# Performance work log

Measured on AMD Instinct MI355X. Metric: run time of the kernel, lower is better.

## Reference

```python
import jax, jax.numpy as jnp
import numpy as np

B, L, D_MODEL = 4, 2048, 256
D_STATE, D_CONV, EXPAND = 16, 4, 2
D_INNER = EXPAND * D_MODEL          # 512
DT_RANK = (D_MODEL + 15) // 16      # 16
HORIZON = 96


def setup_inputs() -> dict:
    key = jax.random.key(0)
    ks = jax.random.split(key, 8)
    s = lambda k, shape, scale=0.02: jax.random.normal(k, shape, dtype=jnp.float32) * scale
    return {
        "x": jax.random.normal(ks[0], (B, L, D_MODEL), dtype=jnp.float32),
        "in_proj_w": s(ks[1], (2 * D_INNER, D_MODEL)),          # no bias (mamba default)
        "conv_w": s(ks[2], (D_INNER, 1, D_CONV), 0.1),          # depthwise causal conv
        "conv_b": jnp.zeros((D_INNER,), jnp.float32),
        "x_proj_w": s(ks[3], (DT_RANK + 2 * D_STATE, D_INNER)),
        "dt_proj_w": s(ks[4], (D_INNER, DT_RANK), 0.1),
        # softplus^{-1}(0.01): typical small initial dt
        "dt_proj_b": jnp.log(jnp.expm1(jnp.full((D_INNER,), 0.01, jnp.float32))),
        "A_log": jnp.log(jnp.broadcast_to(jnp.arange(1, D_STATE + 1, dtype=jnp.float32), (D_INNER, D_STATE))),
        "D_param": jnp.ones((D_INNER,), jnp.float32),
        "out_proj_w": s(ks[5], (D_MODEL, D_INNER)),
        "head_w": s(ks[6], (HORIZON, D_MODEL)),
        "head_b": jnp.zeros((HORIZON,), jnp.float32),
    }


def _silu(x):
    return x * jax.nn.sigmoid(x)


def _forward(x, in_proj_w, conv_w, conv_b, x_proj_w, dt_proj_w, dt_proj_b,
             A_log, D_param, out_proj_w, head_w, head_b):
    # in_proj -> split into conv/ssm branch and gate z
    xz = x @ in_proj_w.T                      # (B, L, 2*d_inner)
    x_in, z = jnp.split(xz, 2, axis=-1)
    # depthwise causal conv over time
    x_t = jnp.transpose(x_in, (0, 2, 1))      # (B, d_inner, L)
    x_conv = jax.lax.conv_general_dilated(
        x_t, conv_w, (1,), [(D_CONV - 1, 0)],
        feature_group_count=D_INNER, dimension_numbers=("NCH", "OIH", "NCH"))
    u = _silu(jnp.transpose(x_conv + conv_b[None, :, None], (0, 2, 1)))  # (B, L, d_inner)
    # input-dependent dt, B, C
    x_dbl = u @ x_proj_w.T
    dt, Bm, Cm = jnp.split(x_dbl, [DT_RANK, DT_RANK + D_STATE], axis=-1)
    delta = jax.nn.softplus(dt @ dt_proj_w.T + dt_proj_b)  # (B, L, d_inner)
    A = -jnp.exp(A_log)                                     # (d_inner, d_state)
    deltaA = jnp.exp(delta[..., None] * A)                  # (B, L, d_inner, d_state)
    deltaBu = delta[..., None] * Bm[:, :, None, :] * u[..., None]

    def step(h, ins):
        dA, dBu, c = ins                                    # (B,d,n),(B,d,n),(B,n)
        h = dA * h + dBu
        y = jnp.einsum("bdn,bn->bd", h, c)
        return h, y

    h0 = jnp.zeros((x.shape[0], D_INNER, D_STATE), x.dtype)
    xs = (jnp.moveaxis(deltaA, 1, 0), jnp.moveaxis(deltaBu, 1, 0), jnp.moveaxis(Cm, 1, 0))
    _, ys = jax.lax.scan(step, h0, xs)                      # (L, B, d_inner)
    y = jnp.moveaxis(ys, 0, 1) + u * D_param
    y = y * _silu(z)
    out = y @ out_proj_w.T                                  # (B, L, d_model)
    last = out[:, -1, :]
    return last @ head_w.T + head_b                         # (B, HORIZON)


def reference(x, in_proj_w, conv_w, conv_b, x_proj_w, dt_proj_w, dt_proj_b,
              A_log, D_param, out_proj_w, head_w, head_b):
    return _forward(x, in_proj_w, conv_w, conv_b, x_proj_w, dt_proj_w, dt_proj_b,
                    A_log, D_param, out_proj_w, head_w, head_b)
```

## Files before the change

### kernel.cpp

```cpp
#include <hip/hip_runtime.h>
#include <math.h>

#define BATCH 4
#define LSEQ 2048
#define BL (BATCH*LSEQ)
#define DMODEL 256
#define DINNER 512
#define NSTATE 16
#define DTRANK 16
#define NPROJ 48
#define HORIZ 96
#define NCH 32
#define TCH (LSEQ/NCH)

typedef __attribute__((ext_vector_type(8))) short short8b;
typedef __attribute__((ext_vector_type(4))) short short4b;
typedef __attribute__((ext_vector_type(4))) float f32x4;

__device__ __forceinline__ unsigned short f2bf(float f) {
  unsigned u = __float_as_uint(f);
  u += 0x7FFF + ((u >> 16) & 1);
  return (unsigned short)(u >> 16);
}
__device__ __forceinline__ float bf2f(unsigned short h) {
  return __uint_as_float(((unsigned)h) << 16);
}

__global__ __launch_bounds__(512) void k_front(const float* __restrict__ X,
                                               const float* __restrict__ W,
                                               const float* __restrict__ cw,
                                               const float* __restrict__ cb,
                                               const float* __restrict__ xpw,
                                               const float* __restrict__ opw,
                                               const float* __restrict__ hw,
                                               float* __restrict__ uT,
                                               float* __restrict__ dbl,
                                               float* __restrict__ hwf) {
  __shared__ unsigned short sBX[32*48*8];
  __shared__ unsigned short sAW[2*4*128*8];
  __shared__ float u_lds[128*36];
  const int tid = threadIdx.x;
  const int btc = blockIdx.x;
  if (btc >= 256) {
    const int fid = btc - 256;
    const int k0 = fid * 8;
    float* scratch = u_lds;
    {
      int m = tid >> 1;
      int half = (tid & 1) << 2;
      *(float4*)&scratch[m * 8 + half] =
        *(const float4*)&opw[(size_t)m * DINNER + k0 + half];
    }
    __syncthreads();
    for (int u = tid; u < HORIZ * 8; u += 512) {
      int t = u >> 3, kk = u & 7;
      const float* hr = &hw[(size_t)t * DMODEL];
      float acc = 0.f;
      #pragma unroll 8
      for (int m = 0; m < DMODEL; ++m) acc = fmaf(hr[m], scratch[m*8 + kk], acc);
      hwf[(size_t)t * DINNER + k0 + kk] = acc;
    }
    return;
  }
  const int bt0 = btc * 32;
  const bool edge0 = ((bt0 & (LSEQ - 1)) == 0);
  const int lane = tid & 63;
  const int w  = tid >> 6;
  const int fl = lane & 15;
  const int fg = lane >> 4;
  for (int u = tid; u < 1536; u += 512) {
    int tok = u >> 5, ko = u & 31;
    int g = bt0 - 16 + tok;
    if (g < 0) g = 0;
    const float* xr = &X[(size_t)g * DMODEL + ko * 8];
    float4 a = *(const float4*)xr, b = *(const float4*)(xr + 4);
    unsigned short t8[8] = {f2bf(a.x), f2bf(a.y), f2bf(a.z), f2bf(a.w),
                            f2bf(b.x), f2bf(b.y), f2bf(b.z), f2bf(b.w)};
    *(short8b*)&sBX[(ko * 48 + tok) * 8] = *(short8b*)t8;
  }
  float facc[4] = {0.f, 0.f, 0.f, 0.f};
  const int xo = tid >> 3;
  const int xt = (tid & 7) * 4;
  const int sj = tid >> 2;
  const int sk = tid & 3;
  for (int jc = 0; jc < 4; ++jc) {
    const int jbase = jc * 128;
    __syncthreads();
    {
      const float* wr = &W[(size_t)(jbase + sj) * DMODEL + sk * 8];
      float4 a = *(const float4*)wr, b = *(const float4*)(wr + 4);
      unsigned short t8[8] = {f2bf(a.x), f2bf(a.y), f2bf(a.z), f2bf(a.w),
                              f2bf(b.x), f2bf(b.y), f2bf(b.z), f2bf(b.w)};
      *(short8b*)&sAW[(sk * 128 + sj) * 8] = *(short8b*)t8;
    }
    __syncthreads();
    f32x4 acc0 = {0,0,0,0}, acc1 = {0,0,0,0}, acc2 = {0,0,0,0};
    for (int ks = 0; ks < 8; ++ks) {
      const int buf = ks & 1;
      if (ks < 7) {
        const float* wr = &W[(size_t)(jbase + sj) * DMODEL + (ks + 1) * 32 + sk * 8];
        float4 a = *(const float4*)wr, b = *(const float4*)(wr + 4);
        unsigned short t8[8] = {f2bf(a.x), f2bf(a.y), f2bf(a.z), f2bf(a.w),
                                f2bf(b.x), f2bf(b.y), f2bf(b.z), f2bf(b.w)};
        *(short8b*)&sAW[((buf ^ 1) * 512 + sk * 128 + sj) * 8] = *(short8b*)t8;
      }
      short8b aw = *(short8b*)&sAW[(buf * 512 + fg * 128 + w * 16 + fl) * 8];
      short8b x0 = *(short8b*)&sBX[((ks * 4 + fg) * 48 + fl) * 8];
      short8b x1 = *(short8b*)&sBX[((ks * 4 + fg) * 48 + 16 + fl) * 8];
      short8b x2 = *(short8b*)&sBX[((ks * 4 + fg) * 48 + 32 + fl) * 8];
      acc0 = __builtin_amdgcn_mfma_f32_16x16x32_bf16(x0, aw, acc0, 0, 0, 0);
      acc1 = __builtin_amdgcn_mfma_f32_16x16x32_bf16(x1, aw, acc1, 0, 0, 0);
      acc2 = __builtin_amdgcn_mfma_f32_16x16x32_bf16(x2, aw, acc2, 0, 0, 0);
      __syncthreads();
    }
    if (edge0) acc0 = (f32x4){0,0,0,0};
    const int j = jbase + w * 16 + fl;
    const float4 cwv = *(const float4*)&cw[j * 4];
    const float cbv = cb[j];
    float u1[4], u2[4];
    {
      float s3a = __shfl(acc1[3], lane - 16), s3b = __shfl(acc0[3], lane + 48);
      float s2a = __shfl(acc1[2], lane - 16), s2b = __shfl(acc0[2], lane + 48);
      float s1a = __shfl(acc1[1], lane - 16), s1b = __shfl(acc0[1], lane + 48);
      float p1 = fg ? s3a : s3b, p2 = fg ? s2a : s2b, p3 = fg ? s1a : s1b;
      float xm1[4] = {p1, acc1[0], acc1[1], acc1[2]};
      float xm2[4] = {p2, p1, acc1[0], acc1[1]};
      float xm3[4] = {p3, p2, p1, acc1[0]};
      #pragma unroll
      for (int r = 0; r < 4; ++r) {
        float s = cbv;
        s = fmaf(cwv.x, xm3[r], s); s = fmaf(cwv.y, xm2[r], s);
        s = fmaf(cwv.z, xm1[r], s); s = fmaf(cwv.w, acc1[r], s);
        u1[r] = s / (1.f + __expf(-s));
      }
    }
    {
      float s3a = __shfl(acc2[3], lane - 16), s3b = __shfl(acc1[3], lane + 48);
      float s2a = __shfl(acc2[2], lane - 16), s2b = __shfl(acc1[2], lane + 48);
      float s1a = __shfl(acc2[1], lane - 16), s1b = __shfl(acc1[1], lane + 48);
      float p1 = fg ? s3a : s3b, p2 = fg ? s2a : s2b, p3 = fg ? s1a : s1b;
      float xm1[4] = {p1, acc2[0], acc2[1], acc2[2]};
      float xm2[4] = {p2, p1, acc2[0], acc2[1]};
      float xm3[4] = {p3, p2, p1, acc2[0]};
      #pragma unroll
      for (int r = 0; r < 4; ++r) {
        float s = cbv;
        s = fmaf(cwv.x, xm3[r], s); s = fmaf(cwv.y, xm2[r], s);
        s = fmaf(cwv.z, xm1[r], s); s = fmaf(cwv.w, acc2[r], s);
        u2[r] = s / (1.f + __expf(-s));
      }
    }
    {
      const int jl = w * 16 + fl;
      #pragma unroll
      for (int r = 0; r < 4; ++r) {
        u_lds[jl * 36 + fg * 4 + r]      = u1[r];
        u_lds[jl * 36 + 16 + fg * 4 + r] = u2[r];
      }
    }
    __syncthreads();
    unsigned short* sw2 = sAW;
    for (int u = tid; u < 1536; u += 512) {
      int o = u >> 5, k4 = (u & 31) * 4;
      float4 v = *(const float4*)&xpw[(size_t)o * DINNER + jbase + k4];
      unsigned short t4[4] = {f2bf(v.x), f2bf(v.y), f2bf(v.z), f2bf(v.w)};
      *(short4b*)&sw2[o * 136 + k4] = *(short4b*)t4;
    }
    {
      const int tq = sk * 8;
      float4 a = *(float4*)&u_lds[sj * 36 + tq];
      float4 b = *(float4*)&u_lds[sj * 36 + tq + 4];
      *(float4*)&uT[(size_t)(jbase + sj) * BL + bt0 + tq]     = a;
      *(float4*)&uT[(size_t)(jbase + sj) * BL + bt0 + tq + 4] = b;
    }
    __syncthreads();
    if (tid < 384) {
      #pragma unroll 4
      for (int k = 0; k < 128; ++k) {
        float wv = bf2f(sw2[xo * 136 + k]);
        float4 uv = *(float4*)&u_lds[k * 36 + xt];
        facc[0] = fmaf(uv.x, wv, facc[0]);
        facc[1] = fmaf(uv.y, wv, facc[1]);
        facc[2] = fmaf(uv.z, wv, facc[2]);
        facc[3] = fmaf(uv.w, wv, facc[3]);
      }
    }
  }
  if (tid < 384) {
    #pragma unroll
    for (int i = 0; i < 4; ++i)
      dbl[(size_t)(bt0 + xt + i) * NPROJ + xo] = facc[i];
  }
}

__global__ __launch_bounds__(256) void k_scan(const float* __restrict__ uT,
                                              const float* __restrict__ dbl,
                                              const float* __restrict__ dtw,
                                              const float* __restrict__ dtb,
                                              const float* __restrict__ Alog,
                                              float* __restrict__ aprod,
                                              float* __restrict__ hacc) {
  __shared__ float sdt[64][17];
  __shared__ float sB[64][16];
  __shared__ float sdp[16][66][2];
  __shared__ float su[16][68];
  __shared__ float sdtw[16][17];
  __shared__ float sdtb[16];
  const int dblk = blockIdx.x, c = blockIdx.y, b = blockIdx.z;
  const int tid = threadIdx.x;
  const int d0 = dblk * 16;
  const int bt0 = b * LSEQ + c * TCH;
  {
    int tok = tid >> 2, q = (tid & 3) << 2;
    float4 v = *(const float4*)&dbl[(size_t)(bt0 + tok) * NPROJ + q];
    sdt[tok][q] = v.x; sdt[tok][q + 1] = v.y; sdt[tok][q + 2] = v.z; sdt[tok][q + 3] = v.w;
    float4 ww = *(const float4*)&dbl[(size_t)(bt0 + tok) * NPROJ + DTRANK + q];
    *(float4*)&sB[tok][q] = ww;
    int dl = tid >> 4, tq = (tid & 15) << 2;
    *(float4*)&su[dl][tq] = *(const float4*)&uT[(size_t)(d0 + dl) * BL + bt0 + tq];
    sdtw[tid >> 4][tid & 15] = dtw[(d0 + (tid >> 4)) * DTRANK + (tid & 15)];
    if (tid < 16) sdtb[tid] = dtb[d0 + tid];
  }
  __syncthreads();
  {
    int tok = tid >> 2, dl4 = (tid & 3) << 2;
    #pragma unroll
    for (int dd = 0; dd < 4; ++dd) {
      int dl = dl4 + dd;
      float a = sdtb[dl];
      #pragma unroll
      for (int r = 0; r < DTRANK; ++r) a = fmaf(sdt[tok][r], sdtw[dl][r], a);
      float dlt = (a > 20.f) ? a : log1pf(__expf(a));
      sdp[dl][tok][0] = dlt;
      sdp[dl][tok][1] = dlt * su[dl][tok];
    }
  }
  __syncthreads();
  const int dl = tid >> 4, n = tid & 15;
  const int d = d0 + dl;
  const float A = -__expf(Alog[d * NSTATE + n]);
  float ap = 1.f, h = 0.f;
  #pragma unroll 8
  for (int tt = 0; tt < TCH; ++tt) {
    float2 dp = *(const float2*)&sdp[dl][tt][0];
    float dA = __expf(dp.x * A);
    h = fmaf(dA, h, dp.y * sB[tt][n]);
    ap *= dA;
  }
  size_t off = (((size_t)b * NCH + c) * DINNER + d) * NSTATE + n;
  aprod[off] = ap;
  hacc[off] = h;
}

__global__ __launch_bounds__(256) void k_combine(const float* __restrict__ aprod,
                                                 const float* __restrict__ hacc,
                                                 const float* __restrict__ dbl,
                                                 const float* __restrict__ uT,
                                                 const float* __restrict__ Dp,
                                                 const float* __restrict__ X,
                                                 const float* __restrict__ ipw,
                                                 float* __restrict__ ybuf) {
  __shared__ float sx[DMODEL];
  const int dblk = blockIdx.x & 31, b = blockIdx.x >> 5;
  const int tid = threadIdx.x;
  const int dl = tid >> 4, n = tid & 15;
  const int d = dblk * 16 + dl;
  sx[tid] = X[((size_t)b * LSEQ + LSEQ - 1) * DMODEL + tid];
  float h = 0.f;
  for (int c = 0; c < NCH; ++c) {
    size_t off = (((size_t)b * NCH + c) * DINNER + d) * NSTATE + n;
    h = fmaf(aprod[off], h, hacc[off]);
  }
  __syncthreads();
  float zp = 0.f;
  {
    const float* zr = &ipw[(size_t)(DINNER + d) * DMODEL + (n << 4)];
    #pragma unroll
    for (int q = 0; q < 4; ++q) {
      float4 w4 = *(const float4*)&zr[q << 2];
      float4 x4 = *(const float4*)&sx[(n << 4) + (q << 2)];
      zp = fmaf(w4.x, x4.x, zp); zp = fmaf(w4.y, x4.y, zp);
      zp = fmaf(w4.z, x4.z, zp); zp = fmaf(w4.w, x4.w, zp);
    }
  }
  const int btL = b * LSEQ + LSEQ - 1;
  float Cv = dbl[(size_t)btL * NPROJ + DTRANK + NSTATE + n];
  float v = h * Cv;
  #pragma unroll
  for (int off = 1; off < 16; off <<= 1) {
    v  += __shfl_xor(v, off);
    zp += __shfl_xor(zp, off);
  }
  if (n == 0) {
    float y = v + uT[(size_t)d * BL + btL] * Dp[d];
    ybuf[b * DINNER + d] = y * zp / (1.f + __expf(-zp));
  }
}

__global__ __launch_bounds__(256) void k_out(const float* __restrict__ sy,
                                             const float* __restrict__ hwf,
                                             const float* __restrict__ hb,
                                             float* __restrict__ out) {
  const int t = blockIdx.x;
  const int b = threadIdx.x >> 6;
  const int lane = threadIdx.x & 63;
  const int k0 = lane << 3;
  const float* yr = &sy[(size_t)b * DINNER + k0];
  const float* wr = &hwf[(size_t)t * DINNER + k0];
  float4 y0 = *(const float4*)yr, y1 = *(const float4*)(yr + 4);
  float4 w0 = *(const float4*)wr, w1 = *(const float4*)(wr + 4);
  float s = y0.x * w0.x + y0.y * w0.y + y0.z * w0.z + y0.w * w0.w
          + y1.x * w1.x + y1.y * w1.y + y1.z * w1.z + y1.w * w1.w;
  #pragma unroll
  for (int off = 1; off < 64; off <<= 1) s += __shfl_xor(s, off);
  if (lane == 0) out[b * HORIZ + t] = s + hb[t];
}

extern "C" void kernel_launch(void* const* d_in, const int* in_sizes, int n_in,
                              void* d_out, int out_size, void* d_ws, size_t ws_size,
                              hipStream_t stream) {
  (void)in_sizes; (void)n_in; (void)out_size; (void)ws_size;
  const float* x    = (const float*)d_in[0];
  const float* ipw  = (const float*)d_in[1];
  const float* cw   = (const float*)d_in[2];
  const float* cb   = (const float*)d_in[3];
  const float* xpw  = (const float*)d_in[4];
  const float* dtw  = (const float*)d_in[5];
  const float* dtb  = (const float*)d_in[6];
  const float* Alog = (const float*)d_in[7];
  const float* Dp   = (const float*)d_in[8];
  const float* opw  = (const float*)d_in[9];
  const float* hw   = (const float*)d_in[10];
  const float* hb   = (const float*)d_in[11];
  float* out = (float*)d_out;
  float* ws  = (float*)d_ws;

  float* uT    = ws;
  float* dbl   = ws + 4194304;
  float* aprod = ws + 4587520;
  float* hacc  = ws + 5636096;
  float* ybuf  = ws + 6684672;
  float* hwf   = ws + 6686720;

  k_front<<<320, 512, 0, stream>>>(x, ipw, cw, cb, xpw, opw, hw, uT, dbl, hwf);
  k_scan<<<dim3(32, NCH, BATCH), 256, 0, stream>>>(uT, dbl, dtw, dtb, Alog, aprod, hacc);
  k_combine<<<128, 256, 0, stream>>>(aprod, hacc, dbl, uT, Dp, x, ipw, ybuf);
  k_out<<<HORIZ, 256, 0, stream>>>(ybuf, hwf, hb, out);
}
```

Measured before the change: 79.95 us.

## Load in_proj weights straight to registers and drop per-k-step LDS barriers

The in_proj weight fragments now go straight from global memory into registers, eight bf16 fragments per lane, and are no longer double-buffered through LDS. That removes the __syncthreads inside the 8-step MFMA loop. The X tile in LDS moves to a token-major padded layout (stride 264), and the x_proj weight staging is hoisted to the start of each chunk into its own LDS buffer, which removes one more barrier. The cost is more VGPR use for the register-held weights and redundant global weight loads across waves, since each wave fetches its own fragment.

Result: faster. 75.62 us (-5.4%).

```diff
diff --git a/kernel.cpp b/kernel.cpp
--- a/kernel.cpp
+++ b/kernel.cpp
@@ -36,9 +36,9 @@
                                                float* __restrict__ uT,
                                                float* __restrict__ dbl,
                                                float* __restrict__ hwf) {
-  __shared__ unsigned short sBX[32*48*8];
-  __shared__ unsigned short sAW[2*4*128*8];
-  __shared__ float u_lds[128*36];
+  __shared__ unsigned short sBX[48 * 264];
+  __shared__ unsigned short sw2[48 * 136];
+  __shared__ float u_lds[128 * 36];
   const int tid = threadIdx.x;
   const int btc = blockIdx.x;
   if (btc >= 256) {
@@ -76,7 +76,7 @@
     float4 a = *(const float4*)xr, b = *(const float4*)(xr + 4);
     unsigned short t8[8] = {f2bf(a.x), f2bf(a.y), f2bf(a.z), f2bf(a.w),
                             f2bf(b.x), f2bf(b.y), f2bf(b.z), f2bf(b.w)};
-    *(short8b*)&sBX[(ko * 48 + tok) * 8] = *(short8b*)t8;
+    *(short8b*)&sBX[tok * 264 + ko * 8] = *(short8b*)t8;
   }
   float facc[4] = {0.f, 0.f, 0.f, 0.f};
   const int xo = tid >> 3;
@@ -86,32 +86,34 @@
   for (int jc = 0; jc < 4; ++jc) {
     const int jbase = jc * 128;
     __syncthreads();
-    {
-      const float* wr = &W[(size_t)(jbase + sj) * DMODEL + sk * 8];
-      float4 a = *(const float4*)wr, b = *(const float4*)(wr + 4);
-      unsigned short t8[8] = {f2bf(a.x), f2bf(a.y), f2bf(a.z), f2bf(a.w),
-                              f2bf(b.x), f2bf(b.y), f2bf(b.z), f2bf(b.w)};
-      *(short8b*)&sAW[(sk * 128 + sj) * 8] = *(short8b*)t8;
-    }
-    __syncthreads();
-    f32x4 acc0 = {0,0,0,0}, acc1 = {0,0,0,0}, acc2 = {0,0,0,0};
-    for (int ks = 0; ks < 8; ++ks) {
-      const int buf = ks & 1;
-      if (ks < 7) {
-        const float* wr = &W[(size_t)(jbase + sj) * DMODEL + (ks + 1) * 32 + sk * 8];
-        float4 a = *(const float4*)wr, b = *(const float4*)(wr + 4);
+    for (int u = tid; u < 1536; u += 512) {
+      int o = u >> 5, k4 = (u & 31) * 4;
+      float4 v = *(const float4*)&xpw[(size_t)o * DINNER + jbase + k4];
+      unsigned short t4[4] = {f2bf(v.x), f2bf(v.y), f2bf(v.z), f2bf(v.w)};
+      *(short4b*)&sw2[o * 136 + k4] = *(short4b*)t4;
+    }
+    short8b aw[8];
+    {
+      const float* wrow = &W[(size_t)(jbase + w * 16 + fl) * DMODEL + fg * 8];
+      #pragma unroll
+      for (int ks = 0; ks < 8; ++ks) {
+        float4 a = *(const float4*)(wrow + ks * 32);
+        float4 b = *(const float4*)(wrow + ks * 32 + 4);
         unsigned short t8[8] = {f2bf(a.x), f2bf(a.y), f2bf(a.z), f2bf(a.w),
                                 f2bf(b.x), f2bf(b.y), f2bf(b.z), f2bf(b.w)};
-        *(short8b*)&sAW[((buf ^ 1) * 512 + sk * 128 + sj) * 8] = *(short8b*)t8;
-      }
-      short8b aw = *(short8b*)&sAW[(buf * 512 + fg * 128 + w * 16 + fl) * 8];
-      short8b x0 = *(short8b*)&sBX[((ks * 4 + fg) * 48 + fl) * 8];
-      short8b x1 = *(short8b*)&sBX[((ks * 4 + fg) * 48 + 16 + fl) * 8];
-      short8b x2 = *(short8b*)&sBX[((ks * 4 + fg) * 48 + 32 + fl) * 8];
-      acc0 = __builtin_amdgcn_mfma_f32_16x16x32_bf16(x0, aw, acc0, 0, 0, 0);
-      acc1 = __builtin_amdgcn_mfma_f32_16x16x32_bf16(x1, aw, acc1, 0, 0, 0);
-      acc2 = __builtin_amdgcn_mfma_f32_16x16x32_bf16(x2, aw, acc2, 0, 0, 0);
-      __syncthreads();
+        aw[ks] = *(short8b*)t8;
+      }
+    }
+    f32x4 acc0 = {0,0,0,0}, acc1 = {0,0,0,0}, acc2 = {0,0,0,0};
+    #pragma unroll
+    for (int ks = 0; ks < 8; ++ks) {
+      const int kcol = (ks * 4 + fg) * 8;
+      short8b x0 = *(short8b*)&sBX[(fl)      * 264 + kcol];
+      short8b x1 = *(short8b*)&sBX[(16 + fl) * 264 + kcol];
+      short8b x2 = *(short8b*)&sBX[(32 + fl) * 264 + kcol];
+      acc0 = __builtin_amdgcn_mfma_f32_16x16x32_bf16(x0, aw[ks], acc0, 0, 0, 0);
+      acc1 = __builtin_amdgcn_mfma_f32_16x16x32_bf16(x1, aw[ks], acc1, 0, 0, 0);
+      acc2 = __builtin_amdgcn_mfma_f32_16x16x32_bf16(x2, aw[ks], acc2, 0, 0, 0);
     }
     if (edge0) acc0 = (f32x4){0,0,0,0};
     const int j = jbase + w * 16 + fl;
@@ -159,13 +161,6 @@
       }
     }
     __syncthreads();
-    unsigned short* sw2 = sAW;
-    for (int u = tid; u < 1536; u += 512) {
-      int o = u >> 5, k4 = (u & 31) * 4;
-      float4 v = *(const float4*)&xpw[(size_t)o * DINNER + jbase + k4];
-      unsigned short t4[4] = {f2bf(v.x), f2bf(v.y), f2bf(v.z), f2bf(v.w)};
-      *(short4b*)&sw2[o * 136 + k4] = *(short4b*)t4;
-    }
     {
       const int tq = sk * 8;
       float4 a = *(float4*)&u_lds[sj * 36 + tq];
@@ -173,7 +168,6 @@
       *(float4*)&uT[(size_t)(jbase + sj) * BL + bt0 + tq]     = a;
       *(float4*)&uT[(size_t)(jbase + sj) * BL + bt0 + tq + 4] = b;
     }
-    __syncthreads();
     if (tid < 384) {
       #pragma unroll 4
       for (int k = 0; k < 128; ++k) {
```
